# Kernel tuning notes

Hardware: AMD Instinct MI355X
Metric: run time of the kernel (lower is better)

Reference implementation:

```python
import jax, jax.numpy as jnp
import numpy as np

EMBED = 512
KDIM = 512
VDIM = 512
HEADS = 8
DHEAD = EMBED // HEADS  # 64
SCALE = 1.0 / np.sqrt(DHEAD).astype(np.float32)


def setup_inputs() -> dict:
    key = jax.random.key(0)
    ks = jax.random.split(key, 11)
    B, Lq, Lk = 4, 2048, 2048
    s_in = 1.0 / np.sqrt(EMBED).astype(np.float32)
    return {
        "query": jax.random.normal(ks[0], (B, Lq, EMBED), jnp.float32),
        "key": jax.random.normal(ks[1], (B, Lk, KDIM), jnp.float32),
        "value": jax.random.normal(ks[2], (B, Lk, VDIM), jnp.float32),
        "wq": jax.random.normal(ks[3], (EMBED, KDIM), jnp.float32) * s_in,
        "bq": jnp.zeros((KDIM,), jnp.float32),
        "wk": jax.random.normal(ks[4], (KDIM, KDIM), jnp.float32) * s_in,
        "bk": jnp.zeros((KDIM,), jnp.float32),
        "wv": jax.random.normal(ks[5], (VDIM, VDIM), jnp.float32) * s_in,
        "bv": jnp.zeros((VDIM,), jnp.float32),
        "wo": jax.random.normal(ks[6], (VDIM, EMBED), jnp.float32) * s_in,
        "bo": jnp.zeros((EMBED,), jnp.float32),
    }


def _split_heads(x):
    b, l, _ = x.shape
    return x.reshape(b, l, HEADS, DHEAD).transpose(0, 2, 1, 3)  # b h l d


def reference(query, key, value, wq, bq, wk, bk, wv, bv, wo, bo):
    # Linear projections (weights stored [in, out])
    q = _split_heads(query @ wq + bq)   # b h Lq d
    k = _split_heads(key @ wk + bk)     # b h Lk d
    v = _split_heads(value @ wv + bv)   # b h Lk d
    scores = jnp.einsum('bhid,bhjd->bhij', q, k) * SCALE  # b h Lq Lk
    attn = jax.nn.softmax(scores, axis=-1)
    # dropout is identity in eval mode
    ctx = jnp.einsum('bhij,bhjd->bhid', attn, v)  # b h Lq d
    b, h, l, d = ctx.shape
    ctx = ctx.transpose(0, 2, 1, 3).reshape(b, l, h * d)  # b Lq vdim
    return ctx @ wo + bo
```

## Files before the change

### kernel.cpp

```cpp
#include <hip/hip_runtime.h>
#include <stdint.h>

typedef unsigned short u16;
typedef unsigned int u32;
typedef __attribute__((ext_vector_type(8))) short short8;
typedef __attribute__((ext_vector_type(4))) float f32x4;
typedef __attribute__((ext_vector_type(16))) float f32x16;

#define DEVI static __device__ __forceinline__

DEVI u16 f2bf(float f) {
  union { float f; u32 u; } v; v.f = f;
  u32 r = v.u + 0x7FFFu + ((v.u >> 16) & 1u);
  return (u16)(r >> 16);
}

DEVI u32 pack2bf(float lo, float hi) {
  return (u32)f2bf(lo) | ((u32)f2bf(hi) << 16);
}

DEVI u32 pack2bf_fast(float lo, float hi) {
  union { float f; u32 u; } a, b;
  a.f = lo; b.f = hi;
  return __builtin_amdgcn_perm(b.u + 0x8000u, a.u + 0x8000u, 0x07060302u);
}

DEVI void gload_lds16(const u16* g, u16* l) {
  __builtin_amdgcn_global_load_lds((const __attribute__((address_space(1))) void*)g,
                                   (__attribute__((address_space(3))) void*)l, 16, 0, 0);
}

DEVI int sw8(int chunk, int r) { return ((chunk ^ (r & 7) ^ ((r >> 3) & 3)) * 8); }

__global__ __launch_bounds__(256) void tw4(const float* __restrict__ s0, const float* __restrict__ s1,
                                           const float* __restrict__ s2, const float* __restrict__ s3,
                                           u16* __restrict__ d0, u16* __restrict__ d1,
                                           u16* __restrict__ d2, u16* __restrict__ d3) {
  int z = blockIdx.z;
  const float* src = z == 0 ? s0 : z == 1 ? s1 : z == 2 ? s2 : s3;
  u16* dst = z == 0 ? d0 : z == 1 ? d1 : z == 2 ? d2 : d3;
  __shared__ float tile[32][33];
  int tx = threadIdx.x & 31, ty = threadIdx.x >> 5;
  int bx = blockIdx.x * 32, by = blockIdx.y * 32;
#pragma unroll
  for (int i = 0; i < 32; i += 8)
    tile[ty + i][tx] = src[(size_t)(by + ty + i) * 512 + bx + tx];
  __syncthreads();
#pragma unroll
  for (int i = 0; i < 32; i += 8)
    dst[(size_t)(bx + ty + i) * 512 + by + tx] = f2bf(tile[tx][ty + i]);
}

__global__ __launch_bounds__(256) void gemm_qkv(
    const float* __restrict__ A0, const float* __restrict__ A1, const float* __restrict__ A2,
    const u16* __restrict__ W0, const u16* __restrict__ W1, const u16* __restrict__ W2,
    const float* __restrict__ b0, const float* __restrict__ b1, const float* __restrict__ b2,
    u16* __restrict__ oq, u16* __restrict__ ok, u16* __restrict__ vt, float qscale) {
  const int z = blockIdx.z;
  const float* A = z == 0 ? A0 : z == 1 ? A1 : A2;
  const u16* WT = z == 0 ? W0 : z == 1 ? W1 : W2;
  const float* bias = z == 0 ? b0 : z == 1 ? b1 : b2;
  const float sc = z == 0 ? qscale : 1.0f;

  __shared__ __align__(16) u16 As[128 * 64];
  __shared__ __align__(16) u16 Bs[128 * 64];
  const int t = threadIdx.x;
  const int w = t >> 6, lane = t & 63, quad = lane >> 4, li = lane & 15;
  const int flat = blockIdx.x + (blockIdx.y << 2);
  const int xcd = flat & 7, idx = flat >> 3;
  const int m0 = (((idx >> 2) << 3) + xcd) * 128;
  const int n0 = (idx & 3) * 128;
  const int wm = (w >> 1) * 64, wn = (w & 1) * 64;

  f32x4 zv = {0.f, 0.f, 0.f, 0.f};
  f32x4 acc[4][4];
#pragma unroll
  for (int mi = 0; mi < 4; mi++)
#pragma unroll
    for (int ni = 0; ni < 4; ni++) acc[mi][ni] = zv;

  const int rA = t >> 3, cA = t & 7;
  for (int it = 0; it < 8; it++) {
    const int k0 = it * 64;
#pragma unroll
    for (int p = 0; p < 4; p++) {
      int r = p * 32 + rA;
      const float* ga = A + (size_t)(m0 + r) * 512 + k0 + cA * 8;
      float4 f0 = *(const float4*)ga;
      float4 f1 = *(const float4*)(ga + 4);
      uint4 pk;
      pk.x = pack2bf_fast(f0.x, f0.y);
      pk.y = pack2bf_fast(f0.z, f0.w);
      pk.z = pack2bf_fast(f1.x, f1.y);
      pk.w = pack2bf_fast(f1.z, f1.w);
      *(uint4*)&As[r * 64 + sw8(cA, r)] = pk;
    }
#pragma unroll
    for (int p = 0; p < 4; p++) {
      int s = p * 256 + t;
      int r = s >> 3, c8 = s & 7;
      gload_lds16(WT + (size_t)(n0 + r) * 512 + k0 + sw8(c8, r), &Bs[(p * 256 + w * 64) * 8]);
    }
    __syncthreads();
#pragma unroll
    for (int ks = 0; ks < 2; ks++) {
      short8 af[4], bf[4];
#pragma unroll
      for (int mi = 0; mi < 4; mi++) {
        int r = wm + mi * 16 + li;
        af[mi] = *(const short8*)&As[r * 64 + sw8(ks * 4 + quad, r)];
      }
#pragma unroll
      for (int ni = 0; ni < 4; ni++) {
        int r = wn + ni * 16 + li;
        bf[ni] = *(const short8*)&Bs[r * 64 + sw8(ks * 4 + quad, r)];
      }
#pragma unroll
      for (int mi = 0; mi < 4; mi++)
#pragma unroll
        for (int ni = 0; ni < 4; ni++)
          acc[mi][ni] = __builtin_amdgcn_mfma_f32_16x16x32_bf16(af[mi], bf[ni], acc[mi][ni], 0, 0, 0);
    }
    __syncthreads();
  }

  float bv[4];
#pragma unroll
  for (int ni = 0; ni < 4; ni++) bv[ni] = bias[n0 + wn + ni * 16 + li];

  if (z < 2) {
    u16* out = z == 0 ? oq : ok;
#pragma unroll
    for (int mi = 0; mi < 4; mi++)
#pragma unroll
      for (int ni = 0; ni < 4; ni++)
#pragma unroll
        for (int r = 0; r < 4; r++) {
          int row = m0 + wm + mi * 16 + quad * 4 + r;
          int col = n0 + wn + ni * 16 + li;
          out[(size_t)row * 512 + col] = f2bf((acc[mi][ni][r] + bv[ni]) * sc);
        }
  } else {
#pragma unroll
    for (int mi = 0; mi < 4; mi++)
#pragma unroll
      for (int ni = 0; ni < 4; ni++) {
        int col = n0 + wn + ni * 16 + li;
        int h = col >> 6, dd = col & 63;
        int row0 = m0 + wm + mi * 16 + quad * 4;
        int bb = row0 >> 11, l0 = row0 & 2047;
        uint2 dw;
        dw.x = pack2bf(acc[mi][ni][0] + bv[ni], acc[mi][ni][1] + bv[ni]);
        dw.y = pack2bf(acc[mi][ni][2] + bv[ni], acc[mi][ni][3] + bv[ni]);
        *(uint2*)&vt[((size_t)((bb * 8 + h) * 64 + dd)) * 2048 + l0] = dw;
      }
  }
}

__global__ __launch_bounds__(256) void gemm_out(const u16* __restrict__ A,
                                                const u16* __restrict__ WT,
                                                const float* __restrict__ bias,
                                                float* __restrict__ out) {
  __shared__ __align__(16) u16 As[128 * 64];
  __shared__ __align__(16) u16 Bs[64 * 64];
  const int t = threadIdx.x;
  const int w = t >> 6, lane = t & 63, quad = lane >> 4, li = lane & 15;
  const int flat = blockIdx.x + (blockIdx.y << 3);
  const int xcd = flat & 7, idx = flat >> 3;
  const int m0 = (((idx >> 3) << 3) + xcd) * 128;
  const int n0 = (idx & 7) * 64;
  const int wm = (w >> 1) * 64, wn = (w & 1) * 32;

  f32x4 zv = {0.f, 0.f, 0.f, 0.f};
  f32x4 acc[4][2];
#pragma unroll
  for (int mi = 0; mi < 4; mi++)
#pragma unroll
    for (int ni = 0; ni < 2; ni++) acc[mi][ni] = zv;

  for (int it = 0; it < 8; it++) {
    const int k0 = it * 64;
#pragma unroll
    for (int p = 0; p < 4; p++) {
      int s = p * 256 + t;
      int r = s >> 3, c8 = s & 7;
      gload_lds16(A + (size_t)(m0 + r) * 512 + k0 + sw8(c8, r), &As[(p * 256 + w * 64) * 8]);
    }
#pragma unroll
    for (int p = 0; p < 2; p++) {
      int s = p * 256 + t;
      int r = s >> 3, c8 = s & 7;
      gload_lds16(WT + (size_t)(n0 + r) * 512 + k0 + sw8(c8, r), &Bs[(p * 256 + w * 64) * 8]);
    }
    __syncthreads();
#pragma unroll
    for (int ks = 0; ks < 2; ks++) {
      short8 af[4], bf[2];
#pragma unroll
      for (int mi = 0; mi < 4; mi++) {
        int r = wm + mi * 16 + li;
        af[mi] = *(const short8*)&As[r * 64 + sw8(ks * 4 + quad, r)];
      }
#pragma unroll
      for (int ni = 0; ni < 2; ni++) {
        int r = wn + ni * 16 + li;
        bf[ni] = *(const short8*)&Bs[r * 64 + sw8(ks * 4 + quad, r)];
      }
#pragma unroll
      for (int mi = 0; mi < 4; mi++)
#pragma unroll
        for (int ni = 0; ni < 2; ni++)
          acc[mi][ni] = __builtin_amdgcn_mfma_f32_16x16x32_bf16(af[mi], bf[ni], acc[mi][ni], 0, 0, 0);
    }
    __syncthreads();
  }

  float bv[2];
#pragma unroll
  for (int ni = 0; ni < 2; ni++) bv[ni] = bias[n0 + wn + ni * 16 + li];
#pragma unroll
  for (int mi = 0; mi < 4; mi++)
#pragma unroll
    for (int ni = 0; ni < 2; ni++)
#pragma unroll
      for (int r = 0; r < 4; r++) {
        int row = m0 + wm + mi * 16 + quad * 4 + r;
        int col = n0 + wn + ni * 16 + li;
        out[(size_t)row * 512 + col] = acc[mi][ni][r] + bv[ni];
      }
}

__global__ __launch_bounds__(256, 4) void attn(const u16* __restrict__ Qp,
                                               const u16* __restrict__ Kp,
                                               const u16* __restrict__ VT,
                                               float* __restrict__ Op,
                                               float* __restrict__ Lb) {
  __shared__ __align__(16) u16 Ks[64 * 64];
  __shared__ __align__(16) u16 Vs[64 * 64];
  __shared__ __align__(16) u16 Ps[4][32 * 64];
  const int t = threadIdx.x;
  const int w = t >> 6, lane = t & 63, qn = lane & 31, hi = lane >> 5;
  const int flat = blockIdx.x + (blockIdx.y << 4);
  const int xcd = flat & 7, idx = flat >> 3;
  const int g = ((idx >> 4) << 3) + xcd;
  const int h = g >> 1, s = g & 1;
  const int b = blockIdx.z;
  const int q0 = (idx & 15) * 128;
  const int qrow = q0 + w * 32 + qn;

  short8 qf[4];
  {
    const u16* qg = Qp + (size_t)(b * 2048 + qrow) * 512 + h * 64 + hi * 8;
#pragma unroll
    for (int ks = 0; ks < 4; ks++) qf[ks] = *(const short8*)(qg + ks * 16);
  }

  f32x16 o[2];
#pragma unroll
  for (int dt = 0; dt < 2; dt++)
#pragma unroll
    for (int r = 0; r < 16; r++) o[dt][r] = 0.f;
  float lsum = 0.f;

  u16* pw = &Ps[w][0];

  for (int kt = s * 16; kt < s * 16 + 16; kt++) {
    const int k0 = kt * 64;
#pragma unroll
    for (int i = 0; i < 2; i++) {
      int si = i * 256 + t;
      int r = si >> 3, c8 = si & 7;
      gload_lds16(Kp + (size_t)(b * 2048 + k0 + r) * 512 + h * 64 + sw8(c8, r),
                  &Ks[(i * 256 + w * 64) * 8]);
      gload_lds16(VT + ((size_t)((b * 8 + h) * 64 + r)) * 2048 + k0 + sw8(c8, r),
                  &Vs[(i * 256 + w * 64) * 8]);
    }
    __syncthreads();

    f32x16 st[2];
#pragma unroll
    for (int kjt = 0; kjt < 2; kjt++) {
#pragma unroll
      for (int r = 0; r < 16; r++) st[kjt][r] = 0.f;
#pragma unroll
      for (int ks = 0; ks < 4; ks++) {
        int m = kjt * 32 + qn;
        short8 ka = *(const short8*)&Ks[m * 64 + sw8(ks * 2 + hi, m)];
        st[kjt] = __builtin_amdgcn_mfma_f32_32x32x16_bf16(ka, qf[ks], st[kjt], 0, 0, 0);
      }
    }

#pragma unroll
    for (int kjt = 0; kjt < 2; kjt++)
#pragma unroll
      for (int k8 = 0; k8 < 4; k8++) {
        float p0 = __builtin_amdgcn_exp2f(st[kjt][k8 * 4 + 0]);
        float p1 = __builtin_amdgcn_exp2f(st[kjt][k8 * 4 + 1]);
        float p2 = __builtin_amdgcn_exp2f(st[kjt][k8 * 4 + 2]);
        float p3 = __builtin_amdgcn_exp2f(st[kjt][k8 * 4 + 3]);
        lsum += (p0 + p1) + (p2 + p3);
        uint2 dw;
        dw.x = pack2bf_fast(p0, p1);
        dw.y = pack2bf_fast(p2, p3);
        *(uint2*)&pw[qn * 64 + sw8(kjt * 4 + k8, qn) + hi * 4] = dw;
      }

    short8 pb[4];
#pragma unroll
    for (int ks = 0; ks < 4; ks++)
      pb[ks] = *(const short8*)&pw[qn * 64 + sw8(ks * 2 + hi, qn)];
#pragma unroll
    for (int dt = 0; dt < 2; dt++)
#pragma unroll
      for (int ks = 0; ks < 4; ks++) {
        int m = dt * 32 + qn;
        short8 va = *(const short8*)&Vs[m * 64 + sw8(ks * 2 + hi, m)];
        o[dt] = __builtin_amdgcn_mfma_f32_32x32x16_bf16(va, pb[ks], o[dt], 0, 0, 0);
      }
    __syncthreads();
  }

  float l = lsum + __shfl_xor(lsum, 32);
  if (hi == 0) Lb[((size_t)((b * 8 + h) * 2 + s)) * 2048 + qrow] = l;
#pragma unroll
  for (int dt = 0; dt < 2; dt++)
#pragma unroll
    for (int r = 0; r < 16; r++) {
      int d = dt * 32 + (r & 3) + 8 * (r >> 2) + 4 * hi;
      Op[((size_t)(((b * 8 + h) * 2 + s) * 64 + d)) * 2048 + qrow] = o[dt][r];
    }
}

__global__ __launch_bounds__(256) void reduce_o(const float* __restrict__ Op,
                                                const float* __restrict__ Lb,
                                                u16* __restrict__ ctx) {
  __shared__ float tile[64 * 65];
  const int t = threadIdx.x;
  const int b = blockIdx.z, h = blockIdx.y, q0 = blockIdx.x * 64;
  {
    int d = t >> 2, qc = (t & 3) * 16;
    const float* p0 = Op + ((size_t)(((b * 8 + h) * 2 + 0) * 64 + d)) * 2048 + q0 + qc;
    const float* p1 = Op + ((size_t)(((b * 8 + h) * 2 + 1) * 64 + d)) * 2048 + q0 + qc;
#pragma unroll
    for (int i = 0; i < 4; i++) {
      float4 a = *(const float4*)(p0 + i * 4);
      float4 c = *(const float4*)(p1 + i * 4);
      float4 v;
      v.x = a.x + c.x; v.y = a.y + c.y; v.z = a.z + c.z; v.w = a.w + c.w;
      *(float4*)&tile[d * 65 + qc + i * 4] = v;
    }
  }
  __syncthreads();
  {
    int q = t >> 2, dc = (t & 3) * 16;
    float l0 = Lb[((size_t)((b * 8 + h) * 2 + 0)) * 2048 + q0 + q];
    float l1 = Lb[((size_t)((b * 8 + h) * 2 + 1)) * 2048 + q0 + q];
    float inv = 1.0f / (l0 + l1);
    u32 pk[8];
#pragma unroll
    for (int i = 0; i < 8; i++) {
      float v0 = tile[(dc + i * 2) * 65 + q] * inv;
      float v1 = tile[(dc + i * 2 + 1) * 65 + q] * inv;
      pk[i] = pack2bf(v0, v1);
    }
    u16* dst = ctx + (size_t)(b * 2048 + q0 + q) * 512 + h * 64 + dc;
    *(uint4*)dst = *(uint4*)&pk[0];
    *(uint4*)(dst + 8) = *(uint4*)&pk[4];
  }
}

extern "C" void kernel_launch(void* const* d_in, const int* in_sizes, int n_in,
                              void* d_out, int out_size, void* d_ws, size_t ws_size,
                              hipStream_t stream) {
  const float* query = (const float*)d_in[0];
  const float* key_ = (const float*)d_in[1];
  const float* value = (const float*)d_in[2];
  const float* wq = (const float*)d_in[3];
  const float* bq = (const float*)d_in[4];
  const float* wk = (const float*)d_in[5];
  const float* bk = (const float*)d_in[6];
  const float* wv = (const float*)d_in[7];
  const float* bv = (const float*)d_in[8];
  const float* wo = (const float*)d_in[9];
  const float* bo = (const float*)d_in[10];

  char* ws = (char*)d_ws;
  const size_t SZ_W = (size_t)512 * 512 * 2;
  const size_t SZ_X = (size_t)8192 * 512 * 2;
  u16* wqT = (u16*)(ws);
  u16* wkT = (u16*)(ws + SZ_W);
  u16* wvT = (u16*)(ws + 2 * SZ_W);
  u16* woT = (u16*)(ws + 3 * SZ_W);
  u16* Qp = (u16*)(ws + 4 * SZ_W);
  u16* Kp = (u16*)(ws + 4 * SZ_W + SZ_X);
  u16* VTp = (u16*)(ws + 4 * SZ_W + 2 * SZ_X);
  float* Opb = (float*)(ws + 4 * SZ_W + 3 * SZ_X);
  float* Lb = (float*)(ws + 4 * SZ_W + 3 * SZ_X + ((size_t)32 << 20));
  u16* ctx = Qp;

  const float C1 = 0.125f * 1.44269504088896f;

  tw4<<<dim3(16, 16, 4), 256, 0, stream>>>(wq, wk, wv, wo, wqT, wkT, wvT, woT);
  gemm_qkv<<<dim3(4, 64, 3), 256, 0, stream>>>(query, key_, value, wqT, wkT, wvT,
                                               bq, bk, bv, Qp, Kp, VTp, C1);
  attn<<<dim3(16, 16, 4), 256, 0, stream>>>(Qp, Kp, VTp, Opb, Lb);
  reduce_o<<<dim3(32, 8, 4), 256, 0, stream>>>(Opb, Lb, ctx);
  gemm_out<<<dim3(8, 64), 256, 0, stream>>>(ctx, woT, bo, (float*)d_out);
}
```

Before: 201.4 us.

## Fuse split-K attention reduction into output GEMM and stage V-transpose via LDS

The attention kernel now writes each split's unnormalized context as bf16 in row-major [token, embed] layout, staged through LDS, instead of fp32 in a transposed layout. The separate reduce_o kernel is removed: gemm_out loads both partial tiles, sums them, applies the per-row 1/(l0+l1) factor and stores the result into LDS as its A operand. The V-transpose epilogue in gemm_qkv is also staged through shared memory so global stores become coalesced 16-byte writes. This drops a launch and fp32 partial traffic. In exchange, gemm_out uses plain loads plus ALU work instead of direct global-to-LDS loads, and the partial sums are rounded to bf16 before they are added.

```diff
diff --git a/kernel.cpp b/kernel.cpp
--- a/kernel.cpp
+++ b/kernel.cpp
@@ -23,6 +23,13 @@
   union { float f; u32 u; } a, b;
   a.f = lo; b.f = hi;
   return __builtin_amdgcn_perm(b.u + 0x8000u, a.u + 0x8000u, 0x07060302u);
+}
+
+DEVI u32 sum2bf(u32 a, u32 b, float sc) {
+  union { u32 u; float f; } alo, ahi, blo, bhi;
+  alo.u = a << 16; ahi.u = a & 0xFFFF0000u;
+  blo.u = b << 16; bhi.u = b & 0xFFFF0000u;
+  return pack2bf_fast((alo.f + blo.f) * sc, (ahi.f + bhi.f) * sc);
 }
 
 DEVI void gload_lds16(const u16* g, u16* l) {
@@ -62,8 +69,9 @@
   const float* bias = z == 0 ? b0 : z == 1 ? b1 : b2;
   const float sc = z == 0 ? qscale : 1.0f;
 
-  __shared__ __align__(16) u16 As[128 * 64];
-  __shared__ __align__(16) u16 Bs[128 * 64];
+  __shared__ __align__(16) u16 smem[128 * 64 * 2];
+  u16* As = smem;
+  u16* Bs = smem + 128 * 64;
   const int t = threadIdx.x;
   const int w = t >> 6, lane = t & 63, quad = lane >> 4, li = lane & 15;
   const int flat = blockIdx.x + (blockIdx.y << 2);
@@ -141,28 +149,41 @@
           out[(size_t)row * 512 + col] = f2bf((acc[mi][ni][r] + bv[ni]) * sc);
         }
   } else {
+    u16* LT = smem;
 #pragma unroll
     for (int mi = 0; mi < 4; mi++)
 #pragma unroll
       for (int ni = 0; ni < 4; ni++) {
-        int col = n0 + wn + ni * 16 + li;
-        int h = col >> 6, dd = col & 63;
-        int row0 = m0 + wm + mi * 16 + quad * 4;
-        int bb = row0 >> 11, l0 = row0 & 2047;
+        int col = wn + ni * 16 + li;
+        int row0 = wm + mi * 16 + quad * 4;
         uint2 dw;
         dw.x = pack2bf(acc[mi][ni][0] + bv[ni], acc[mi][ni][1] + bv[ni]);
         dw.y = pack2bf(acc[mi][ni][2] + bv[ni], acc[mi][ni][3] + bv[ni]);
-        *(uint2*)&vt[((size_t)((bb * 8 + h) * 64 + dd)) * 2048 + l0] = dw;
-      }
-  }
-}
-
-__global__ __launch_bounds__(256) void gemm_out(const u16* __restrict__ A,
+        *(uint2*)&LT[col * 128 + (row0 ^ ((col & 7) << 3))] = dw;
+      }
+    __syncthreads();
+    const int rr = t >> 1, half = t & 1;
+    const int colg = n0 + rr;
+    const int h = colg >> 6, dd = colg & 63;
+    const int bb = m0 >> 11, l0 = m0 & 2047;
+    u16* gdst = vt + ((size_t)((bb * 8 + h) * 64 + dd)) * 2048 + l0 + half * 64;
+#pragma unroll
+    for (int c = 0; c < 8; c++) {
+      short8 v = *(const short8*)&LT[rr * 128 + half * 64 + ((c ^ (rr & 7)) << 3)];
+      *(short8*)(gdst + c * 8) = v;
+    }
+  }
+}
+
+__global__ __launch_bounds__(256) void gemm_out(const u16* __restrict__ O0,
+                                                const u16* __restrict__ O1,
+                                                const float* __restrict__ Lb,
                                                 const u16* __restrict__ WT,
                                                 const float* __restrict__ bias,
                                                 float* __restrict__ out) {
   __shared__ __align__(16) u16 As[128 * 64];
   __shared__ __align__(16) u16 Bs[64 * 64];
+  __shared__ float Linv[8 * 128];
   const int t = threadIdx.x;
   const int w = t >> 6, lane = t & 63, quad = lane >> 4, li = lane & 15;
   const int flat = blockIdx.x + (blockIdx.y << 3);
@@ -170,6 +191,17 @@
   const int m0 = (((idx >> 3) << 3) + xcd) * 128;
   const int n0 = (idx & 7) * 64;
   const int wm = (w >> 1) * 64, wn = (w & 1) * 32;
+  const int bb = m0 >> 11, qb = m0 & 2047;
+
+#pragma unroll
+  for (int j = 0; j < 4; j++) {
+    int f2 = t + j * 256;
+    int hh = f2 >> 7, qq = f2 & 127;
+    float l0v = Lb[((size_t)((bb * 8 + hh) * 2 + 0)) * 2048 + qb + qq];
+    float l1v = Lb[((size_t)((bb * 8 + hh) * 2 + 1)) * 2048 + qb + qq];
+    Linv[f2] = 1.0f / (l0v + l1v);
+  }
+  __syncthreads();
 
   f32x4 zv = {0.f, 0.f, 0.f, 0.f};
   f32x4 acc[4][2];
@@ -178,13 +210,22 @@
 #pragma unroll
     for (int ni = 0; ni < 2; ni++) acc[mi][ni] = zv;
 
+  const int rA = t >> 3, cA = t & 7;
   for (int it = 0; it < 8; it++) {
     const int k0 = it * 64;
 #pragma unroll
     for (int p = 0; p < 4; p++) {
-      int s = p * 256 + t;
-      int r = s >> 3, c8 = s & 7;
-      gload_lds16(A + (size_t)(m0 + r) * 512 + k0 + sw8(c8, r), &As[(p * 256 + w * 64) * 8]);
+      int r = p * 32 + rA;
+      size_t off = (size_t)(m0 + r) * 512 + k0 + cA * 8;
+      uint4 a0 = *(const uint4*)&O0[off];
+      uint4 a1 = *(const uint4*)&O1[off];
+      float scq = Linv[it * 128 + r];
+      uint4 pk;
+      pk.x = sum2bf(a0.x, a1.x, scq);
+      pk.y = sum2bf(a0.y, a1.y, scq);
+      pk.z = sum2bf(a0.z, a1.z, scq);
+      pk.w = sum2bf(a0.w, a1.w, scq);
+      *(uint4*)&As[r * 64 + sw8(cA, r)] = pk;
     }
 #pragma unroll
     for (int p = 0; p < 2; p++) {
@@ -233,7 +274,8 @@
 __global__ __launch_bounds__(256, 4) void attn(const u16* __restrict__ Qp,
                                                const u16* __restrict__ Kp,
                                                const u16* __restrict__ VT,
-                                               float* __restrict__ Op,
+                                               u16* __restrict__ Oq0,
+                                               u16* __restrict__ Oq1,
                                                float* __restrict__ Lb) {
   __shared__ __align__(16) u16 Ks[64 * 64];
   __shared__ __align__(16) u16 Vs[64 * 64];
@@ -322,50 +364,23 @@
 
   float l = lsum + __shfl_xor(lsum, 32);
   if (hi == 0) Lb[((size_t)((b * 8 + h) * 2 + s)) * 2048 + qrow] = l;
+  u16* Oq = s == 0 ? Oq0 : Oq1;
 #pragma unroll
   for (int dt = 0; dt < 2; dt++)
 #pragma unroll
-    for (int r = 0; r < 16; r++) {
-      int d = dt * 32 + (r & 3) + 8 * (r >> 2) + 4 * hi;
-      Op[((size_t)(((b * 8 + h) * 2 + s) * 64 + d)) * 2048 + qrow] = o[dt][r];
-    }
-}
-
-__global__ __launch_bounds__(256) void reduce_o(const float* __restrict__ Op,
-                                                const float* __restrict__ Lb,
-                                                u16* __restrict__ ctx) {
-  __shared__ float tile[64 * 65];
-  const int t = threadIdx.x;
-  const int b = blockIdx.z, h = blockIdx.y, q0 = blockIdx.x * 64;
-  {
-    int d = t >> 2, qc = (t & 3) * 16;
-    const float* p0 = Op + ((size_t)(((b * 8 + h) * 2 + 0) * 64 + d)) * 2048 + q0 + qc;
-    const float* p1 = Op + ((size_t)(((b * 8 + h) * 2 + 1) * 64 + d)) * 2048 + q0 + qc;
-#pragma unroll
-    for (int i = 0; i < 4; i++) {
-      float4 a = *(const float4*)(p0 + i * 4);
-      float4 c = *(const float4*)(p1 + i * 4);
-      float4 v;
-      v.x = a.x + c.x; v.y = a.y + c.y; v.z = a.z + c.z; v.w = a.w + c.w;
-      *(float4*)&tile[d * 65 + qc + i * 4] = v;
-    }
-  }
-  __syncthreads();
-  {
-    int q = t >> 2, dc = (t & 3) * 16;
-    float l0 = Lb[((size_t)((b * 8 + h) * 2 + 0)) * 2048 + q0 + q];
-    float l1 = Lb[((size_t)((b * 8 + h) * 2 + 1)) * 2048 + q0 + q];
-    float inv = 1.0f / (l0 + l1);
-    u32 pk[8];
-#pragma unroll
-    for (int i = 0; i < 8; i++) {
-      float v0 = tile[(dc + i * 2) * 65 + q] * inv;
-      float v1 = tile[(dc + i * 2 + 1) * 65 + q] * inv;
-      pk[i] = pack2bf(v0, v1);
-    }
-    u16* dst = ctx + (size_t)(b * 2048 + q0 + q) * 512 + h * 64 + dc;
-    *(uint4*)dst = *(uint4*)&pk[0];
-    *(uint4*)(dst + 8) = *(uint4*)&pk[4];
+    for (int k8 = 0; k8 < 4; k8++) {
+      uint2 dw;
+      dw.x = pack2bf_fast(o[dt][k8 * 4 + 0], o[dt][k8 * 4 + 1]);
+      dw.y = pack2bf_fast(o[dt][k8 * 4 + 2], o[dt][k8 * 4 + 3]);
+      *(uint2*)&pw[qn * 64 + sw8(dt * 4 + k8, qn) + hi * 4] = dw;
+    }
+  __builtin_amdgcn_s_waitcnt(0);
+  int q = lane >> 1, half = lane & 1;
+  u16* dst = Oq + (size_t)(b * 2048 + q0 + w * 32 + q) * 512 + h * 64 + half * 32;
+#pragma unroll
+  for (int cc = 0; cc < 4; cc++) {
+    int chunk = half * 4 + cc;
+    *(short8*)(dst + cc * 8) = *(const short8*)&pw[q * 64 + sw8(chunk, q)];
   }
 }
 
@@ -394,16 +409,15 @@
   u16* Qp = (u16*)(ws + 4 * SZ_W);
   u16* Kp = (u16*)(ws + 4 * SZ_W + SZ_X);
   u16* VTp = (u16*)(ws + 4 * SZ_W + 2 * SZ_X);
-  float* Opb = (float*)(ws + 4 * SZ_W + 3 * SZ_X);
-  float* Lb = (float*)(ws + 4 * SZ_W + 3 * SZ_X + ((size_t)32 << 20));
-  u16* ctx = Qp;
+  u16* Oq0 = (u16*)(ws + 4 * SZ_W + 3 * SZ_X);
+  u16* Oq1 = (u16*)(ws + 4 * SZ_W + 4 * SZ_X);
+  float* Lb = (float*)(ws + 4 * SZ_W + 5 * SZ_X);
 
   const float C1 = 0.125f * 1.44269504088896f;
 
   tw4<<<dim3(16, 16, 4), 256, 0, stream>>>(wq, wk, wv, wo, wqT, wkT, wvT, woT);
   gemm_qkv<<<dim3(4, 64, 3), 256, 0, stream>>>(query, key_, value, wqT, wkT, wvT,
                                                bq, bk, bv, Qp, Kp, VTp, C1);
-  attn<<<dim3(16, 16, 4), 256, 0, stream>>>(Qp, Kp, VTp, Opb, Lb);
-  reduce_o<<<dim3(32, 8, 4), 256, 0, stream>>>(Opb, Lb, ctx);
-  gemm_out<<<dim3(8, 64), 256, 0, stream>>>(ctx, woT, bo, (float*)d_out);
-}
+  attn<<<dim3(16, 16, 4), 256, 0, stream>>>(Qp, Kp, VTp, Oq0, Oq1, Lb);
+  gemm_out<<<dim3(8, 64), 256, 0, stream>>>(Oq0, Oq1, Lb, woT, bo, (float*)d_out);
+}
```

After: 199.6 us. No clear change (-0.9%).
